# Kernel tuning notes

Measured on AMD Instinct MI355X. Metric: run time of the kernel, lower is better.

Reference implementation:

```python
import jax, jax.numpy as jnp
import numpy as np

EPS_KERNEL = 1e-4   # eps added inside softmax_kernel exp
EPS_DENOM = 1e-6    # eps added to k_cumsum in the denominator
N_CHUNKS = 128      # matches torch.chunk(128, dim=-2) in causal_linear_attention_noncuda


def gaussian_orthogonal_random_matrix(nb_rows, nb_cols, rng):
    # scaling=0: rows are orthogonal blocks scaled by chi-distributed norms
    n_full = nb_rows // nb_cols + (1 if nb_rows % nb_cols else 0)
    blocks = []
    for _ in range(n_full):
        g = rng.standard_normal((nb_cols, nb_cols))
        qmat, _ = np.linalg.qr(g)
        blocks.append(qmat.T)
    mat = np.concatenate(blocks, axis=0)[:nb_rows]
    multiplier = np.linalg.norm(rng.standard_normal((nb_rows, nb_cols)), axis=1)
    return (multiplier[:, None] * mat).astype(np.float32)


def softmax_kernel(x, proj, is_query):
    # x: [b,h,n,d], proj: [m,d] -> phi(x): [b,h,n,m]
    d = x.shape[-1]
    normalizer = d ** -0.25
    ratio = proj.shape[0] ** -0.5
    xd = jnp.einsum('bhnd,md->bhnm', normalizer * x, proj)
    diag = 0.5 * (normalizer ** 2) * jnp.sum(x * x, axis=-1, keepdims=True)  # [b,h,n,1]
    if is_query:
        mx = jnp.max(xd, axis=-1, keepdims=True)
    else:
        mx = jnp.max(xd, axis=(-1, -2), keepdims=True)
    return ratio * (jnp.exp(xd - diag - mx) + EPS_KERNEL)


def causal_linear_attention(q, k, v):
    # q,k: [b,h,n,m] phi-features; v: [b,h,n,d]
    b, h, n, m = q.shape
    d = v.shape[-1]
    c = n // N_CHUNKS  # chunk length

    def chunked(t):
        return jnp.moveaxis(t.reshape(b, h, N_CHUNKS, c, t.shape[-1]), 2, 0)

    qc, kc, vc = chunked(q), chunked(k), chunked(v)  # [nc,b,h,c,*]

    def step(carry, inp):
        k_last, ctx_last = carry  # [b,h,m], [b,h,m,d]
        qi, ki, vi = inp
        k_cum = k_last[:, :, None, :] + jnp.cumsum(ki, axis=2)            # [b,h,c,m]
        d_inv = 1.0 / jnp.einsum('bhcm,bhcm->bhc', qi, k_cum + EPS_DENOM)
        ctx = jnp.einsum('bhcm,bhcd->bhcmd', ki, vi)                      # [b,h,c,m,d]
        ctx_cum = ctx_last[:, :, None, :, :] + jnp.cumsum(ctx, axis=2)
        out = jnp.einsum('bhcmd,bhcm,bhc->bhcd', ctx_cum, qi, d_inv)
        return (k_cum[:, :, -1], ctx_cum[:, :, -1]), out

    init = (jnp.zeros((b, h, m), q.dtype), jnp.zeros((b, h, m, d), q.dtype))
    _, outs = jax.lax.scan(jax.checkpoint(step), init, (qc, kc, vc))
    return jnp.moveaxis(outs, 0, 2).reshape(b, h, n, d)


def setup_inputs() -> dict:
    key = jax.random.key(0)
    kq, kk, kv = jax.random.split(key, 3)
    shape = (2, 8, 2048, 64)  # [batch, heads, seq, dim_heads]
    q = jax.random.normal(kq, shape, dtype=jnp.float32)
    k = jax.random.normal(kk, shape, dtype=jnp.float32)
    v = jax.random.normal(kv, shape, dtype=jnp.float32)
    proj = jnp.asarray(gaussian_orthogonal_random_matrix(256, 64, np.random.default_rng(0)))
    return {"q": q, "k": k, "v": v, "projection_matrix": proj}


def reference(q, k, v, projection_matrix):
    q_prime = softmax_kernel(q, projection_matrix, is_query=True)
    k_prime = softmax_kernel(k, projection_matrix, is_query=False)
    return causal_linear_attention(q_prime, k_prime, v)
```

## Files before the change

### kernel.cpp

```cpp
#include <hip/hip_runtime.h>
#include <hip/hip_bf16.h>
#include <cstddef>

typedef __attribute__((ext_vector_type(8))) short bf16x8;
typedef __attribute__((ext_vector_type(4))) float f32x4;

#define NCH_ 512
#define NRM_ 0.35355339059327373f
#define RATIO_ 0.0625f
#define EPSC_ 6.25e-6f
#define MFMA(a,b,c) __builtin_amdgcn_mfma_f32_16x16x32_bf16((a),(b),(c),0,0,0)

__device__ __forceinline__ unsigned short f2b(float f) {
  unsigned u = __float_as_uint(f);
  u += 0x7FFFu + ((u >> 16) & 1u);
  return (unsigned short)(u >> 16);
}
__device__ __forceinline__ float b2f(unsigned short h) {
  return __uint_as_float(((unsigned)h) << 16);
}
__device__ __forceinline__ unsigned pk2f(float a, float b) {
  union { __hip_bfloat162 h; unsigned u; } cv;
  cv.h = __float22bfloat162_rn(make_float2(a, b));
  return cv.u;
}
__device__ __forceinline__ float sumsq4(float4 a){ return a.x*a.x+a.y*a.y+a.z*a.z+a.w*a.w; }

__global__ __launch_bounds__(256, 2) void kfeat_kernel(
    const float* __restrict__ kg, const float* __restrict__ vg,
    const float* __restrict__ projg,
    unsigned short* __restrict__ kvxP,
    float* __restrict__ blockmax, float* __restrict__ vsumG)
{
  __shared__ unsigned short R0[256*72];
  __shared__ unsigned short XB[128*72];
  __shared__ unsigned short C_[80*72];
  __shared__ float diagS[64];
  __shared__ float rmS[4];
  const int t=threadIdx.x, ch=blockIdx.x;
  const int row0 = ch*64;
  const int lane=t&63, m16=lane&15, q4=lane>>4, w=t>>6;
  const int f0 = w*64;
  unsigned short* kpS = R0;
  unsigned short* xbS = XB;
  unsigned short* kpT = XB;

#pragma unroll
  for (int i=0;i<8;++i){ int flat=i*2048+t*8; int f=flat>>6, d2=flat&63;
    float4 p0 = *(const float4*)(projg+flat);
    float4 p1 = *(const float4*)(projg+flat+4);
    *(uint4*)&R0[f*72+d2] = make_uint4(pk2f(p0.x,p0.y),pk2f(p0.z,p0.w),
                                       pk2f(p1.x,p1.y),pk2f(p1.z,p1.w)); }
  {
    const float* xg = kg + (size_t)row0*64;
#pragma unroll
    for (int i=0;i<4;++i){
      int flat=i*1024+t*4; int r=flat>>6, d2=flat&63;
      float4 f = *(const float4*)(xg+flat);
      float ss = sumsq4(f);
      ss += __shfl_xor(ss,1); ss += __shfl_xor(ss,2);
      ss += __shfl_xor(ss,4); ss += __shfl_xor(ss,8);
      if ((t&15)==0) diagS[r] = 0.0625f*ss;
      *(uint2*)&xbS[r*72+d2] = make_uint2(pk2f(NRM_*f.x,NRM_*f.y), pk2f(NRM_*f.z,NRM_*f.w));
    }
  }
  {
    int c = t&63, sq_ = t>>6;
#pragma unroll
    for (int i=0;i<16;++i)
      C_[c*72 + sq_*16 + i] = f2b(vg[((size_t)row0 + sq_*16 + i)*64 + c]);
    int cc = 64 + (t>>4), s4 = (t&15)*4;
    unsigned short hv = (cc==64) ? (unsigned short)0x3F80 : (unsigned short)0;
    unsigned pv = (unsigned)hv | ((unsigned)hv<<16);
    *(uint2*)&C_[cc*72 + s4] = make_uint2(pv, pv);
  }
  __syncthreads();

  if (t < 80) {
    float s = 0.f;
#pragma unroll 16
    for (int i=0;i<64;++i) s += b2f(C_[t*72+i]);
    vsumG[(size_t)ch*80 + t] = s;
  }

  bf16x8 b[4][2]; float diag4[4];
#pragma unroll
  for (int rt=0;rt<4;++rt){
    b[rt][0] = *(const bf16x8*)&xbS[(rt*16+m16)*72 + q4*8];
    b[rt][1] = *(const bf16x8*)&xbS[(rt*16+m16)*72 + 32 + q4*8];
    diag4[rt] = diagS[rt*16+m16];
  }
  f32x4 acc[4][4];
#pragma unroll
  for (int rt=0;rt<4;++rt)
#pragma unroll
    for (int mt=0;mt<4;++mt) acc[rt][mt] = (f32x4){0.f,0.f,0.f,0.f};
#pragma unroll
  for (int kk=0;kk<2;++kk)
#pragma unroll
    for (int mt=0;mt<4;++mt){
      bf16x8 a = *(const bf16x8*)&R0[(f0+mt*16+m16)*72 + kk*32 + q4*8];
#pragma unroll
      for (int rt=0;rt<4;++rt)
        acc[rt][mt] = MFMA(a, b[rt][kk], acc[rt][mt]);
    }
  {
    float mx = acc[0][0][0];
#pragma unroll
    for (int rt=0;rt<4;++rt)
#pragma unroll
      for (int mt=0;mt<4;++mt)
#pragma unroll
        for (int j=0;j<4;++j) mx = fmaxf(mx, acc[rt][mt][j]);
#pragma unroll
    for (int off=1; off<64; off<<=1) mx = fmaxf(mx, __shfl_xor(mx, off));
    if (lane == 0) rmS[w] = mx;
  }
  __syncthreads();
  const float cmax = fmaxf(fmaxf(rmS[0],rmS[1]),fmaxf(rmS[2],rmS[3]));
  if (t == 0) blockmax[ch] = cmax;

  unsigned kpx[4][4][2];
#pragma unroll
  for (int rt=0;rt<4;++rt){
    float e = diag4[rt] + cmax;
    int rr = rt*16+m16;
#pragma unroll
    for (int mt=0;mt<4;++mt){
      float v0 = RATIO_*__expf(acc[rt][mt][0]-e);
      float v1 = RATIO_*__expf(acc[rt][mt][1]-e);
      float v2 = RATIO_*__expf(acc[rt][mt][2]-e);
      float v3 = RATIO_*__expf(acc[rt][mt][3]-e);
      kpx[rt][mt][0] = pk2f(v0,v1); kpx[rt][mt][1] = pk2f(v2,v3);
      *(uint2*)&kpS[rr*264 + f0 + mt*16 + q4*4] = make_uint2(kpx[rt][mt][0], kpx[rt][mt][1]);
    }
  }
  if ((w>>1) == 0) {
#pragma unroll
    for (int rt=0;rt<4;++rt)
#pragma unroll
      for (int mt=0;mt<4;++mt)
#pragma unroll
        for (int jp=0;jp<2;++jp){
          int frl = (w&1)*64 + mt*16 + q4*4 + jp*2;
          unsigned uv = kpx[rt][mt][jp];
          kpT[frl*72 + rt*16+m16]     = (unsigned short)uv;
          kpT[(frl+1)*72 + rt*16+m16] = (unsigned short)(uv>>16);
        }
  }
  __syncthreads();
#pragma unroll
  for (int h=0; h<2; ++h) {
    if (h == 1) {
      __syncthreads();
      if ((w>>1) == 1) {
#pragma unroll
        for (int rt=0;rt<4;++rt)
#pragma unroll
          for (int mt=0;mt<4;++mt)
#pragma unroll
            for (int jp=0;jp<2;++jp){
              int frl = (w&1)*64 + mt*16 + q4*4 + jp*2;
              unsigned uv = kpx[rt][mt][jp];
              kpT[frl*72 + rt*16+m16]     = (unsigned short)uv;
              kpT[(frl+1)*72 + rt*16+m16] = (unsigned short)(uv>>16);
            }
      }
      __syncthreads();
    }
    f32x4 c2a[5][2];
#pragma unroll
    for (int ct=0;ct<5;++ct)
#pragma unroll
      for (int p=0;p<2;++p) c2a[ct][p] = (f32x4){0.f,0.f,0.f,0.f};
#pragma unroll
    for (int kk=0;kk<2;++kk){
      bf16x8 av[5];
#pragma unroll
      for (int ct=0;ct<5;++ct)
        av[ct] = *(const bf16x8*)&C_[(ct*16+m16)*72 + kk*32 + q4*8];
#pragma unroll
      for (int p=0;p<2;++p){
        int mtl = w*2 + p;
        bf16x8 bv = *(const bf16x8*)&kpT[(mtl*16+m16)*72 + kk*32 + q4*8];
#pragma unroll
        for (int ct=0;ct<5;++ct)
          c2a[ct][p] = MFMA(av[ct], bv, c2a[ct][p]);
      }
    }
#pragma unroll
    for (int ct=0;ct<5;++ct)
#pragma unroll
      for (int p=0;p<2;++p){
        int mtg = h*8 + w*2 + p;
        int mrow = mtg*16 + m16;
        int fb = (mrow>>5)*512 + ((mrow>>3)&3)*8 + (mrow&7);
        unsigned short* dst = kvxP + (size_t)(ch*5+ct)*4096 + fb + (q4*4)*32;
#pragma unroll
        for (int j=0;j<4;++j)
          dst[j*32] = f2b(c2a[ct][p][j]);
      }
    if (h == 0) __syncthreads();
  }
}

__global__ __launch_bounds__(256, 4) void scan_kernel(
    const unsigned short* __restrict__ kvxP, unsigned short* __restrict__ sxP,
    const float* __restrict__ blockmax, const float* __restrict__ vsumG)
{
  __shared__ float sS[32];
  __shared__ float vsS[32][16];
  const int t = threadIdx.x, bid = blockIdx.x;
  const int qtr = bid & 3, ct = (bid>>2)%5, bh = bid/20;
  if (t < 32) {
    float bm = blockmax[bh*32 + t];
    float km = bm;
#pragma unroll
    for (int off=16; off>=1; off>>=1) km = fmaxf(km, __shfl_xor(km, off));
    sS[t] = __expf(bm - km);
  }
  for (int i=t; i<512; i+=256){
    int chl = i>>4, c16 = i&15;
    vsS[chl][c16] = vsumG[(size_t)(bh*32+chl)*80 + ct*16 + c16];
  }
  __syncthreads();
  const int fbase = qtr*1024 + t*4;
  const int c16t = (t>>3)&15;
  const bool isEps = (ct==4) && (c16t == 1);
  float carry0=0.f, carry1=0.f, carry2=0.f, carry3=0.f;
  const size_t stride = (size_t)5*4096;
  size_t base = ((size_t)(bh*32)*5 + ct)*4096 + fbase;
#pragma unroll 4
  for (int chl=0; chl<32; ++chl){
    unsigned s0, s1;
    if (isEps) { unsigned ee = pk2f(1e-6f,1e-6f); s0 = ee; s1 = ee; }
    else { s0 = pk2f(carry0,carry1); s1 = pk2f(carry2,carry3); }
    *(uint2*)(sxP + base) = make_uint2(s0, s1);
    uint2 raw = *(const uint2*)(kvxP + base);
    float sch = sS[chl];
    float evs = EPSC_ * vsS[chl][c16t];
    carry0 += sch*b2f((unsigned short)(raw.x))     + evs;
    carry1 += sch*b2f((unsigned short)(raw.x>>16)) + evs;
    carry2 += sch*b2f((unsigned short)(raw.y))     + evs;
    carry3 += sch*b2f((unsigned short)(raw.y>>16)) + evs;
    base += stride;
  }
}

__global__ __launch_bounds__(256, 2) void out_kernel(
    const float* __restrict__ qg, const float* __restrict__ kg,
    const float* __restrict__ projg, const unsigned short* __restrict__ sxP,
    const float* __restrict__ vg, const float* __restrict__ blockmax,
    float* __restrict__ out_g)
{
  __shared__ unsigned short R0[256*72];
  __shared__ unsigned short KX[64*72];
  __shared__ unsigned short QX[64*72];
  __shared__ unsigned short C_[80*72];
  __shared__ float diagK[64];
  __shared__ float diagQ[64];
  __shared__ float rmS[4*64];
  __shared__ float cmS[4];
  __shared__ float schS;
  const int t=threadIdx.x, ch=blockIdx.x;
  const int row0 = ch*64;
  const int lane=t&63, m16=lane&15, q4=lane>>4, w=t>>6;
  const int f0 = w*64, r0 = w*16;
  unsigned short* P = KX;

#pragma unroll
  for (int i=0;i<8;++i){ int flat=i*2048+t*8; int f=flat>>6, d2=flat&63;
    float4 p0 = *(const float4*)(projg+flat);
    float4 p1 = *(const float4*)(projg+flat+4);
    *(uint4*)&R0[f*72+d2] = make_uint4(pk2f(p0.x,p0.y),pk2f(p0.z,p0.w),
                                       pk2f(p1.x,p1.y),pk2f(p1.z,p1.w)); }
  {
    const float* xg = kg + (size_t)row0*64;
#pragma unroll
    for (int i=0;i<4;++i){
      int flat=i*1024+t*4; int r=flat>>6, d2=flat&63;
      float4 f = *(const float4*)(xg+flat);
      float ss = sumsq4(f);
      ss += __shfl_xor(ss,1); ss += __shfl_xor(ss,2);
      ss += __shfl_xor(ss,4); ss += __shfl_xor(ss,8);
      if ((t&15)==0) diagK[r] = 0.0625f*ss;
      *(uint2*)&KX[r*72+d2] = make_uint2(pk2f(NRM_*f.x,NRM_*f.y), pk2f(NRM_*f.z,NRM_*f.w));
    }
  }
  {
    const float* xg = qg + (size_t)row0*64;
#pragma unroll
    for (int i=0;i<4;++i){
      int flat=i*1024+t*4; int r=flat>>6, d2=flat&63;
      float4 f = *(const float4*)(xg+flat);
      float ss = sumsq4(f);
      ss += __shfl_xor(ss,1); ss += __shfl_xor(ss,2);
      ss += __shfl_xor(ss,4); ss += __shfl_xor(ss,8);
      if ((t&15)==0) diagQ[r] = 0.0625f*ss;
      *(uint2*)&QX[r*72+d2] = make_uint2(pk2f(NRM_*f.x,NRM_*f.y), pk2f(NRM_*f.z,NRM_*f.w));
    }
  }
  {
    int c = t&63, sq_ = t>>6;
#pragma unroll
    for (int i=0;i<16;++i)
      C_[c*72 + sq_*16 + i] = f2b(vg[((size_t)row0 + sq_*16 + i)*64 + c]);
    int cc = 64 + (t>>4), s4 = (t&15)*4;
    unsigned short hv = (cc==64) ? (unsigned short)0x3F80 : (unsigned short)0;
    unsigned pv = (unsigned)hv | ((unsigned)hv<<16);
    *(uint2*)&C_[cc*72 + s4] = make_uint2(pv, pv);
  }
  if (t < 32) {
    float bm = blockmax[(ch>>5)*32 + t];
    float km = bm;
#pragma unroll
    for (int off=16; off>=1; off>>=1) km = fmaxf(km, __shfl_xor(km, off));
    if (t == (ch & 31)) schS = __expf(bm - km);
  }
  __syncthreads();

  bf16x8 bk[4][2], bq[4][2]; float dk4[4], dq4[4];
#pragma unroll
  for (int rt=0;rt<4;++rt){
    bk[rt][0] = *(const bf16x8*)&KX[(rt*16+m16)*72 + q4*8];
    bk[rt][1] = *(const bf16x8*)&KX[(rt*16+m16)*72 + 32 + q4*8];
    bq[rt][0] = *(const bf16x8*)&QX[(rt*16+m16)*72 + q4*8];
    bq[rt][1] = *(const bf16x8*)&QX[(rt*16+m16)*72 + 32 + q4*8];
    dk4[rt] = diagK[rt*16+m16];
    dq4[rt] = diagQ[rt*16+m16];
  }
  f32x4 kacc[4][4], qacc[4][4];
#pragma unroll
  for (int rt=0;rt<4;++rt)
#pragma unroll
    for (int mt=0;mt<4;++mt){ kacc[rt][mt] = (f32x4){0.f,0.f,0.f,0.f};
                              qacc[rt][mt] = (f32x4){0.f,0.f,0.f,0.f}; }
#pragma unroll
  for (int kk=0;kk<2;++kk)
#pragma unroll
    for (int mt=0;mt<4;++mt){
      bf16x8 a = *(const bf16x8*)&R0[(f0+mt*16+m16)*72 + kk*32 + q4*8];
#pragma unroll
      for (int rt=0;rt<4;++rt){
        kacc[rt][mt] = MFMA(a, bk[rt][kk], kacc[rt][mt]);
        qacc[rt][mt] = MFMA(a, bq[rt][kk], qacc[rt][mt]);
      }
    }
  {
    float mx = kacc[0][0][0];
#pragma unroll
    for (int rt=0;rt<4;++rt)
#pragma unroll
      for (int mt=0;mt<4;++mt)
#pragma unroll
        for (int j=0;j<4;++j) mx = fmaxf(mx, kacc[rt][mt][j]);
#pragma unroll
    for (int off=1; off<64; off<<=1) mx = fmaxf(mx, __shfl_xor(mx, off));
    if (lane == 0) cmS[w] = mx;
  }
#pragma unroll
  for (int rt=0;rt<4;++rt){
    float p = qacc[rt][0][0];
#pragma unroll
    for (int mt=0;mt<4;++mt)
#pragma unroll
      for (int j=0;j<4;++j) p = fmaxf(p, qacc[rt][mt][j]);
    p = fmaxf(p, __shfl_xor(p,16)); p = fmaxf(p, __shfl_xor(p,32));
    if (q4 == 0) rmS[w*64 + rt*16+m16] = p;
  }
  __syncthreads();
  const float cmax = fmaxf(fmaxf(cmS[0],cmS[1]),fmaxf(cmS[2],cmS[3]));

  unsigned short* qS = R0;
#pragma unroll
  for (int rt=0;rt<4;++rt){
    int rr = rt*16+m16;
    float rm = fmaxf(fmaxf(rmS[rr],rmS[64+rr]),fmaxf(rmS[128+rr],rmS[192+rr]));
    float e = dq4[rt] + rm;
#pragma unroll
    for (int mt=0;mt<4;++mt){
      float v0 = RATIO_*(__expf(qacc[rt][mt][0]-e)+1e-4f);
      float v1 = RATIO_*(__expf(qacc[rt][mt][1]-e)+1e-4f);
      float v2 = RATIO_*(__expf(qacc[rt][mt][2]-e)+1e-4f);
      float v3 = RATIO_*(__expf(qacc[rt][mt][3]-e)+1e-4f);
      *(uint2*)&qS[rr*264 + f0 + mt*16 + q4*4] = make_uint2(pk2f(v0,v1), pk2f(v2,v3));
    }
  }
  __syncthreads();
  bf16x8 aq[8];
#pragma unroll
  for (int kk=0;kk<8;++kk)
    aq[kk] = *(const bf16x8*)&qS[(r0+m16)*264 + kk*32 + q4*8];
  float q1v = 0.f;
#pragma unroll
  for (int kk=0;kk<8;++kk){
    union { bf16x8 v; unsigned u[4]; } av; av.v = aq[kk];
#pragma unroll
    for (int i=0;i<4;++i)
      q1v += b2f((unsigned short)av.u[i]) + b2f((unsigned short)(av.u[i]>>16));
  }
  q1v += __shfl_xor(q1v,16); q1v += __shfl_xor(q1v,32);
  __syncthreads();

  unsigned short* kpS = R0;
#pragma unroll
  for (int rt=0;rt<4;++rt){
    float e = dk4[rt] + cmax;
    int rr = rt*16+m16;
#pragma unroll
    for (int mt=0;mt<4;++mt){
      float v0 = RATIO_*__expf(kacc[rt][mt][0]-e);
      float v1 = RATIO_*__expf(kacc[rt][mt][1]-e);
      float v2 = RATIO_*__expf(kacc[rt][mt][2]-e);
      float v3 = RATIO_*__expf(kacc[rt][mt][3]-e);
      *(uint2*)&kpS[rr*264 + f0 + mt*16 + q4*4] = make_uint2(pk2f(v0,v1), pk2f(v2,v3));
    }
  }
  __syncthreads();

  f32x4 accA[4], accO[5];
#pragma unroll
  for (int i=0;i<4;++i) accA[i] = (f32x4){0.f,0.f,0.f,0.f};
#pragma unroll
  for (int i=0;i<5;++i) accO[i] = (f32x4){0.f,0.f,0.f,0.f};
  const unsigned short* sxb = sxP + (size_t)ch*5*4096 + m16*32 + q4*8;
#pragma unroll
  for (int kk=0;kk<8;++kk){
    bf16x8 a = aq[kk];
#pragma unroll
    for (int st=0;st<4;++st){
      bf16x8 bfr = *(const bf16x8*)&kpS[(st*16+m16)*264 + kk*32 + q4*8];
      accA[st] = MFMA(a, bfr, accA[st]);
    }
#pragma unroll
    for (int ct=0;ct<5;++ct)
      accO[ct] = MFMA(a, *(const bf16x8*)(sxb + (size_t)ct*4096 + kk*512), accO[ct]);
  }
  __syncthreads();
  const float sch = schS;
#pragma unroll
  for (int j=0;j<4;++j){
    int rr = r0 + q4*4 + j;
    float q1r = __shfl(q1v, q4*4 + j);
    float addc = EPSC_ * q1r;
#pragma unroll
    for (int st=0;st<4;++st){
      int cc = st*16 + m16;
      P[rr*72 + cc] = f2b((cc<=rr) ? (sch*accA[st][j] + addc) : 0.f);
    }
  }
#pragma unroll
  for (int k2=0;k2<2;++k2){
    bf16x8 aP = *(const bf16x8*)&P[(r0+m16)*72 + k2*32 + q4*8];
#pragma unroll
    for (int ct=0;ct<5;++ct){
      bf16x8 bfr = *(const bf16x8*)&C_[(ct*16+m16)*72 + k2*32 + q4*8];
      accO[ct] = MFMA(aP, bfr, accO[ct]);
    }
  }
  __syncthreads();
  float* oT = (float*)R0;
#pragma unroll
  for (int j=0;j<4;++j){
    float d64 = __shfl(accO[4][j], (lane & 48));
    float d65 = __shfl(accO[4][j], (lane & 48) | 1);
    float dinv = 1.f/(d64+d65);
    int rr = r0 + q4*4 + j;
#pragma unroll
    for (int ct=0;ct<4;++ct)
      oT[rr*68 + ct*16 + m16] = accO[ct][j]*dinv;
  }
  __syncthreads();
#pragma unroll
  for (int i=0;i<4;++i){ int flat=i*1024+t*4; int r=flat>>6, c2=flat&63;
    *(float4*)(out_g + (size_t)row0*64 + flat) = *(const float4*)&oT[r*68+c2]; }
}

extern "C" void kernel_launch(void* const* d_in, const int* in_sizes, int n_in,
                              void* d_out, int out_size, void* d_ws, size_t ws_size,
                              hipStream_t stream)
{
  (void)in_sizes; (void)n_in; (void)out_size; (void)ws_size;
  const float* q    = (const float*)d_in[0];
  const float* k    = (const float*)d_in[1];
  const float* v    = (const float*)d_in[2];
  const float* proj = (const float*)d_in[3];
  float* out = (float*)d_out;

  char* p8 = (char*)d_ws;
  unsigned short* kvxP = (unsigned short*)p8; p8 += (size_t)NCH_*5*4096*2;
  unsigned short* sxP  = (unsigned short*)p8; p8 += (size_t)NCH_*5*4096*2;
  float* blockmax = (float*)p8; p8 += NCH_*sizeof(float);
  float* vsumG    = (float*)p8;

  kfeat_kernel<<<dim3(NCH_), dim3(256), 0, stream>>>(k, v, proj, kvxP,
                                                     blockmax, vsumG);
  scan_kernel <<<dim3(320),  dim3(256), 0, stream>>>(kvxP, sxP, blockmax, vsumG);
  out_kernel  <<<dim3(NCH_), dim3(256), 0, stream>>>(q, k, proj, sxP, v,
                                                     blockmax, out);
}
```

Before: 114.7 us.

## Fuse feature, scan and output kernels into one persistent kernel with grid barriers

Replaces the three-kernel pipeline (k-features, chunk scan, output) with a single kernel of 512 blocks that synchronises through atomic-counter grid barriers. Each block keeps its q/k features, V tile and kp tile in shared memory across phases, so the output phase no longer recomputes projections or reloads inputs. The aim is to remove the launch gaps and the redundant recomputation between kernels. It relies on all 512 blocks being co-resident (checked with an occupancy query, with the old path kept as fallback), adds a memset per call, and spends time spinning at the barriers.

```diff
diff --git a/kernel.cpp b/kernel.cpp
--- a/kernel.cpp
+++ b/kernel.cpp
@@ -25,6 +25,370 @@
   return cv.u;
 }
 __device__ __forceinline__ float sumsq4(float4 a){ return a.x*a.x+a.y*a.y+a.z*a.z+a.w*a.w; }
+
+__device__ __forceinline__ void gbar(unsigned* cnt, unsigned goal) {
+  __syncthreads();
+  if (threadIdx.x == 0) {
+    __threadfence();
+    __hip_atomic_fetch_add(cnt, 1u, __ATOMIC_RELEASE, __HIP_MEMORY_SCOPE_AGENT);
+    while (__hip_atomic_fetch_add(cnt, 0u, __ATOMIC_RELAXED, __HIP_MEMORY_SCOPE_AGENT) < goal)
+      __builtin_amdgcn_s_sleep(2);
+    __threadfence();
+  }
+  __syncthreads();
+}
+
+__global__ __launch_bounds__(256, 2) void fused_kernel(
+    const float* __restrict__ qg, const float* __restrict__ kg,
+    const float* __restrict__ vg, const float* __restrict__ projg,
+    unsigned short* __restrict__ kvxP, unsigned short* __restrict__ sxP,
+    float* __restrict__ blockmax, float* __restrict__ vsumG,
+    float* __restrict__ out_g, unsigned* __restrict__ barcnt)
+{
+  __shared__ unsigned short R0[256*72];
+  __shared__ unsigned short XB[128*72];
+  __shared__ unsigned short C_[80*72];
+  __shared__ float diagK[64];
+  __shared__ float diagQ[64];
+  __shared__ float rmS[4*64];
+  __shared__ float cmS[4];
+  __shared__ float schS;
+  const int t=threadIdx.x, ch=blockIdx.x;
+  const int row0 = ch*64;
+  const int lane=t&63, m16=lane&15, q4=lane>>4, w=t>>6;
+  const int f0 = w*64, r0 = w*16;
+  unsigned short* KX = XB;
+  unsigned short* QX = XB + 64*72;
+  unsigned short* kpT = XB;
+
+#pragma unroll
+  for (int i=0;i<8;++i){ int flat=i*2048+t*8; int f=flat>>6, d2=flat&63;
+    float4 p0 = *(const float4*)(projg+flat);
+    float4 p1 = *(const float4*)(projg+flat+4);
+    *(uint4*)&R0[f*72+d2] = make_uint4(pk2f(p0.x,p0.y),pk2f(p0.z,p0.w),
+                                       pk2f(p1.x,p1.y),pk2f(p1.z,p1.w)); }
+  {
+    const float* xg = kg + (size_t)row0*64;
+#pragma unroll
+    for (int i=0;i<4;++i){
+      int flat=i*1024+t*4; int r=flat>>6, d2=flat&63;
+      float4 f = *(const float4*)(xg+flat);
+      float ss = sumsq4(f);
+      ss += __shfl_xor(ss,1); ss += __shfl_xor(ss,2);
+      ss += __shfl_xor(ss,4); ss += __shfl_xor(ss,8);
+      if ((t&15)==0) diagK[r] = 0.0625f*ss;
+      *(uint2*)&KX[r*72+d2] = make_uint2(pk2f(NRM_*f.x,NRM_*f.y), pk2f(NRM_*f.z,NRM_*f.w));
+    }
+  }
+  {
+    const float* xg = qg + (size_t)row0*64;
+#pragma unroll
+    for (int i=0;i<4;++i){
+      int flat=i*1024+t*4; int r=flat>>6, d2=flat&63;
+      float4 f = *(const float4*)(xg+flat);
+      float ss = sumsq4(f);
+      ss += __shfl_xor(ss,1); ss += __shfl_xor(ss,2);
+      ss += __shfl_xor(ss,4); ss += __shfl_xor(ss,8);
+      if ((t&15)==0) diagQ[r] = 0.0625f*ss;
+      *(uint2*)&QX[r*72+d2] = make_uint2(pk2f(NRM_*f.x,NRM_*f.y), pk2f(NRM_*f.z,NRM_*f.w));
+    }
+  }
+  {
+    int c = t&63, sq_ = t>>6;
+#pragma unroll
+    for (int i=0;i<16;++i)
+      C_[c*72 + sq_*16 + i] = f2b(vg[((size_t)row0 + sq_*16 + i)*64 + c]);
+    int cc = 64 + (t>>4), s4 = (t&15)*4;
+    unsigned short hv = (cc==64) ? (unsigned short)0x3F80 : (unsigned short)0;
+    unsigned pv = (unsigned)hv | ((unsigned)hv<<16);
+    *(uint2*)&C_[cc*72 + s4] = make_uint2(pv, pv);
+  }
+  __syncthreads();
+
+  if (t < 80) {
+    float s = 0.f;
+#pragma unroll 16
+    for (int i=0;i<64;++i) s += b2f(C_[t*72+i]);
+    vsumG[(size_t)ch*80 + t] = s;
+  }
+
+  bf16x8 bk[4][2], bq[4][2]; float dk4[4], dq4[4];
+#pragma unroll
+  for (int rt=0;rt<4;++rt){
+    bk[rt][0] = *(const bf16x8*)&KX[(rt*16+m16)*72 + q4*8];
+    bk[rt][1] = *(const bf16x8*)&KX[(rt*16+m16)*72 + 32 + q4*8];
+    bq[rt][0] = *(const bf16x8*)&QX[(rt*16+m16)*72 + q4*8];
+    bq[rt][1] = *(const bf16x8*)&QX[(rt*16+m16)*72 + 32 + q4*8];
+    dk4[rt] = diagK[rt*16+m16];
+    dq4[rt] = diagQ[rt*16+m16];
+  }
+  f32x4 kacc[4][4], qacc[4][4];
+#pragma unroll
+  for (int rt=0;rt<4;++rt)
+#pragma unroll
+    for (int mt=0;mt<4;++mt){ kacc[rt][mt] = (f32x4){0.f,0.f,0.f,0.f};
+                              qacc[rt][mt] = (f32x4){0.f,0.f,0.f,0.f}; }
+#pragma unroll
+  for (int kk=0;kk<2;++kk)
+#pragma unroll
+    for (int mt=0;mt<4;++mt){
+      bf16x8 a = *(const bf16x8*)&R0[(f0+mt*16+m16)*72 + kk*32 + q4*8];
+#pragma unroll
+      for (int rt=0;rt<4;++rt){
+        kacc[rt][mt] = MFMA(a, bk[rt][kk], kacc[rt][mt]);
+        qacc[rt][mt] = MFMA(a, bq[rt][kk], qacc[rt][mt]);
+      }
+    }
+  {
+    float mx = kacc[0][0][0];
+#pragma unroll
+    for (int rt=0;rt<4;++rt)
+#pragma unroll
+      for (int mt=0;mt<4;++mt)
+#pragma unroll
+        for (int j=0;j<4;++j) mx = fmaxf(mx, kacc[rt][mt][j]);
+#pragma unroll
+    for (int off=1; off<64; off<<=1) mx = fmaxf(mx, __shfl_xor(mx, off));
+    if (lane == 0) cmS[w] = mx;
+  }
+#pragma unroll
+  for (int rt=0;rt<4;++rt){
+    float p = qacc[rt][0][0];
+#pragma unroll
+    for (int mt=0;mt<4;++mt)
+#pragma unroll
+      for (int j=0;j<4;++j) p = fmaxf(p, qacc[rt][mt][j]);
+    p = fmaxf(p, __shfl_xor(p,16)); p = fmaxf(p, __shfl_xor(p,32));
+    if (q4 == 0) rmS[w*64 + rt*16+m16] = p;
+  }
+  __syncthreads();
+  const float cmax = fmaxf(fmaxf(cmS[0],cmS[1]),fmaxf(cmS[2],cmS[3]));
+  if (t == 0) blockmax[ch] = cmax;
+
+  unsigned short* qS = R0;
+#pragma unroll
+  for (int rt=0;rt<4;++rt){
+    int rr = rt*16+m16;
+    float rm = fmaxf(fmaxf(rmS[rr],rmS[64+rr]),fmaxf(rmS[128+rr],rmS[192+rr]));
+    float e = dq4[rt] + rm;
+#pragma unroll
+    for (int mt=0;mt<4;++mt){
+      float v0 = RATIO_*(__expf(qacc[rt][mt][0]-e)+1e-4f);
+      float v1 = RATIO_*(__expf(qacc[rt][mt][1]-e)+1e-4f);
+      float v2 = RATIO_*(__expf(qacc[rt][mt][2]-e)+1e-4f);
+      float v3 = RATIO_*(__expf(qacc[rt][mt][3]-e)+1e-4f);
+      *(uint2*)&qS[rr*264 + f0 + mt*16 + q4*4] = make_uint2(pk2f(v0,v1), pk2f(v2,v3));
+    }
+  }
+  __syncthreads();
+  bf16x8 aq[8];
+#pragma unroll
+  for (int kk=0;kk<8;++kk)
+    aq[kk] = *(const bf16x8*)&qS[(r0+m16)*264 + kk*32 + q4*8];
+  float q1v = 0.f;
+#pragma unroll
+  for (int kk=0;kk<8;++kk){
+    union { bf16x8 v; unsigned u[4]; } av; av.v = aq[kk];
+#pragma unroll
+    for (int i=0;i<4;++i)
+      q1v += b2f((unsigned short)av.u[i]) + b2f((unsigned short)(av.u[i]>>16));
+  }
+  q1v += __shfl_xor(q1v,16); q1v += __shfl_xor(q1v,32);
+  __syncthreads();
+
+  unsigned short* kpS = R0;
+  unsigned kpx[4][4][2];
+#pragma unroll
+  for (int rt=0;rt<4;++rt){
+    float e = dk4[rt] + cmax;
+    int rr = rt*16+m16;
+#pragma unroll
+    for (int mt=0;mt<4;++mt){
+      float v0 = RATIO_*__expf(kacc[rt][mt][0]-e);
+      float v1 = RATIO_*__expf(kacc[rt][mt][1]-e);
+      float v2 = RATIO_*__expf(kacc[rt][mt][2]-e);
+      float v3 = RATIO_*__expf(kacc[rt][mt][3]-e);
+      kpx[rt][mt][0] = pk2f(v0,v1); kpx[rt][mt][1] = pk2f(v2,v3);
+      *(uint2*)&kpS[rr*264 + f0 + mt*16 + q4*4] = make_uint2(kpx[rt][mt][0], kpx[rt][mt][1]);
+    }
+  }
+  if ((w>>1) == 0) {
+#pragma unroll
+    for (int rt=0;rt<4;++rt)
+#pragma unroll
+      for (int mt=0;mt<4;++mt)
+#pragma unroll
+        for (int jp=0;jp<2;++jp){
+          int frl = (w&1)*64 + mt*16 + q4*4 + jp*2;
+          unsigned uv = kpx[rt][mt][jp];
+          kpT[frl*72 + rt*16+m16]     = (unsigned short)uv;
+          kpT[(frl+1)*72 + rt*16+m16] = (unsigned short)(uv>>16);
+        }
+  }
+  __syncthreads();
+#pragma unroll
+  for (int h=0; h<2; ++h) {
+    if (h == 1) {
+      __syncthreads();
+      if ((w>>1) == 1) {
+#pragma unroll
+        for (int rt=0;rt<4;++rt)
+#pragma unroll
+          for (int mt=0;mt<4;++mt)
+#pragma unroll
+            for (int jp=0;jp<2;++jp){
+              int frl = (w&1)*64 + mt*16 + q4*4 + jp*2;
+              unsigned uv = kpx[rt][mt][jp];
+              kpT[frl*72 + rt*16+m16]     = (unsigned short)uv;
+              kpT[(frl+1)*72 + rt*16+m16] = (unsigned short)(uv>>16);
+            }
+      }
+      __syncthreads();
+    }
+    f32x4 c2a[5][2];
+#pragma unroll
+    for (int ct=0;ct<5;++ct)
+#pragma unroll
+      for (int p=0;p<2;++p) c2a[ct][p] = (f32x4){0.f,0.f,0.f,0.f};
+#pragma unroll
+    for (int kk=0;kk<2;++kk){
+      bf16x8 av[5];
+#pragma unroll
+      for (int ct=0;ct<5;++ct)
+        av[ct] = *(const bf16x8*)&C_[(ct*16+m16)*72 + kk*32 + q4*8];
+#pragma unroll
+      for (int p=0;p<2;++p){
+        int mtl = w*2 + p;
+        bf16x8 bv = *(const bf16x8*)&kpT[(mtl*16+m16)*72 + kk*32 + q4*8];
+#pragma unroll
+        for (int ct=0;ct<5;++ct)
+          c2a[ct][p] = MFMA(av[ct], bv, c2a[ct][p]);
+      }
+    }
+#pragma unroll
+    for (int ct=0;ct<5;++ct)
+#pragma unroll
+      for (int p=0;p<2;++p){
+        int mtg = h*8 + w*2 + p;
+        int mrow = mtg*16 + m16;
+        int fb = (mrow>>5)*512 + ((mrow>>3)&3)*8 + (mrow&7);
+        unsigned short* dst = kvxP + (size_t)(ch*5+ct)*4096 + fb + (q4*4)*32;
+#pragma unroll
+        for (int j=0;j<4;++j)
+          dst[j*32] = f2b(c2a[ct][p][j]);
+      }
+    if (h == 0) __syncthreads();
+  }
+
+  gbar(barcnt, (unsigned)gridDim.x);
+
+  if (t < 32) {
+    float bm = blockmax[(ch>>5)*32 + t];
+    float km = bm;
+#pragma unroll
+    for (int off=16; off>=1; off>>=1) km = fmaxf(km, __shfl_xor(km, off));
+    if (t == (ch & 31)) schS = __expf(bm - km);
+  }
+  if (ch < 320) {
+    float* sS  = (float*)XB;
+    float* vsS = ((float*)XB) + 32;
+    const int qtr = ch & 3, ct5 = (ch>>2)%5, bh = ch/20;
+    if (t < 32) {
+      float bm = blockmax[bh*32 + t];
+      float km = bm;
+#pragma unroll
+      for (int off=16; off>=1; off>>=1) km = fmaxf(km, __shfl_xor(km, off));
+      sS[t] = __expf(bm - km);
+    }
+    for (int i=t; i<512; i+=256){
+      int chl = i>>4, c16 = i&15;
+      vsS[chl*16+c16] = vsumG[(size_t)(bh*32+chl)*80 + ct5*16 + c16];
+    }
+    __syncthreads();
+    const int fbase = qtr*1024 + t*4;
+    const int c16t = (t>>3)&15;
+    const bool isEps = (ct5==4) && (c16t == 1);
+    float carry0=0.f, carry1=0.f, carry2=0.f, carry3=0.f;
+    const size_t stride = (size_t)5*4096;
+    size_t base = ((size_t)(bh*32)*5 + ct5)*4096 + fbase;
+#pragma unroll 4
+    for (int chl=0; chl<32; ++chl){
+      unsigned s0, s1;
+      if (isEps) { unsigned ee = pk2f(1e-6f,1e-6f); s0 = ee; s1 = ee; }
+      else { s0 = pk2f(carry0,carry1); s1 = pk2f(carry2,carry3); }
+      *(uint2*)(sxP + base) = make_uint2(s0, s1);
+      uint2 raw = *(const uint2*)(kvxP + base);
+      float sc_ = sS[chl];
+      float evs = EPSC_ * vsS[chl*16+c16t];
+      carry0 += sc_*b2f((unsigned short)(raw.x))     + evs;
+      carry1 += sc_*b2f((unsigned short)(raw.x>>16)) + evs;
+      carry2 += sc_*b2f((unsigned short)(raw.y))     + evs;
+      carry3 += sc_*b2f((unsigned short)(raw.y>>16)) + evs;
+      base += stride;
+    }
+  }
+
+  gbar(barcnt, 2u*(unsigned)gridDim.x);
+
+  f32x4 accA[4], accO[5];
+#pragma unroll
+  for (int i=0;i<4;++i) accA[i] = (f32x4){0.f,0.f,0.f,0.f};
+#pragma unroll
+  for (int i=0;i<5;++i) accO[i] = (f32x4){0.f,0.f,0.f,0.f};
+  const unsigned short* sxb = sxP + (size_t)ch*5*4096 + m16*32 + q4*8;
+#pragma unroll
+  for (int kk=0;kk<8;++kk){
+    bf16x8 a = aq[kk];
+#pragma unroll
+    for (int st=0;st<4;++st){
+      bf16x8 bfr = *(const bf16x8*)&kpS[(st*16+m16)*264 + kk*32 + q4*8];
+      accA[st] = MFMA(a, bfr, accA[st]);
+    }
+#pragma unroll
+    for (int ct=0;ct<5;++ct)
+      accO[ct] = MFMA(a, *(const bf16x8*)(sxb + (size_t)ct*4096 + kk*512), accO[ct]);
+  }
+  __syncthreads();
+  const float sch = schS;
+  unsigned short* P = XB;
+#pragma unroll
+  for (int j=0;j<4;++j){
+    int rr = r0 + q4*4 + j;
+    float q1r = __shfl(q1v, q4*4 + j);
+    float addc = EPSC_ * q1r;
+#pragma unroll
+    for (int st=0;st<4;++st){
+      int cc = st*16 + m16;
+      P[rr*72 + cc] = f2b((cc<=rr) ? (sch*accA[st][j] + addc) : 0.f);
+    }
+  }
+#pragma unroll
+  for (int k2=0;k2<2;++k2){
+    bf16x8 aP = *(const bf16x8*)&P[(r0+m16)*72 + k2*32 + q4*8];
+#pragma unroll
+    for (int ct=0;ct<5;++ct){
+      bf16x8 bfr = *(const bf16x8*)&C_[(ct*16+m16)*72 + k2*32 + q4*8];
+      accO[ct] = MFMA(aP, bfr, accO[ct]);
+    }
+  }
+  __syncthreads();
+  float* oT = (float*)R0;
+#pragma unroll
+  for (int j=0;j<4;++j){
+    float d64 = __shfl(accO[4][j], (lane & 48));
+    float d65 = __shfl(accO[4][j], (lane & 48) | 1);
+    float dinv = 1.f/(d64+d65);
+    int rr = r0 + q4*4 + j;
+#pragma unroll
+    for (int ct=0;ct<4;++ct)
+      oT[rr*68 + ct*16 + m16] = accO[ct][j]*dinv;
+  }
+  __syncthreads();
+#pragma unroll
+  for (int i=0;i<4;++i){ int flat=i*1024+t*4; int r=flat>>6, c2=flat&63;
+    *(float4*)(out_g + (size_t)row0*64 + flat) = *(const float4*)&oT[r*68+c2]; }
+}
+
 
 __global__ __launch_bounds__(256, 2) void kfeat_kernel(
     const float* __restrict__ kg, const float* __restrict__ vg,
@@ -491,11 +855,26 @@
   unsigned short* kvxP = (unsigned short*)p8; p8 += (size_t)NCH_*5*4096*2;
   unsigned short* sxP  = (unsigned short*)p8; p8 += (size_t)NCH_*5*4096*2;
   float* blockmax = (float*)p8; p8 += NCH_*sizeof(float);
-  float* vsumG    = (float*)p8;
-
-  kfeat_kernel<<<dim3(NCH_), dim3(256), 0, stream>>>(k, v, proj, kvxP,
-                                                     blockmax, vsumG);
-  scan_kernel <<<dim3(320),  dim3(256), 0, stream>>>(kvxP, sxP, blockmax, vsumG);
-  out_kernel  <<<dim3(NCH_), dim3(256), 0, stream>>>(q, k, proj, sxP, v,
-                                                     blockmax, out);
+  float* vsumG    = (float*)p8; p8 += (size_t)NCH_*80*sizeof(float);
+  unsigned* barcnt = (unsigned*)p8;
+
+  static int fused_ok = -1;
+  if (fused_ok < 0) {
+    int nb = 0;
+    hipError_t e = hipOccupancyMaxActiveBlocksPerMultiprocessor(&nb, fused_kernel,
+                                                                256, (size_t)0);
+    fused_ok = (e == hipSuccess && nb >= 2) ? 1 : 0;
+  }
+
+  if (fused_ok) {
+    hipMemsetAsync(barcnt, 0, sizeof(unsigned), stream);
+    fused_kernel<<<dim3(NCH_), dim3(256), 0, stream>>>(q, k, v, proj, kvxP, sxP,
+                                                       blockmax, vsumG, out, barcnt);
+  } else {
+    kfeat_kernel<<<dim3(NCH_), dim3(256), 0, stream>>>(k, v, proj, kvxP,
+                                                       blockmax, vsumG);
+    scan_kernel <<<dim3(320),  dim3(256), 0, stream>>>(kvxP, sxP, blockmax, vsumG);
+    out_kernel  <<<dim3(NCH_), dim3(256), 0, stream>>>(q, k, proj, sxP, v,
+                                                       blockmax, out);
+  }
 }
```

After: 115.2 us. About the same (+0.4%).
